# Kernel optimization log

Measured on AMD Instinct MI355X. Metric: run time of the kernel, lower is better.

The kernel has to match this reference:

```python
import jax, jax.numpy as jnp
import numpy as np

EPS = 0.1        # entropic regularization (self.eps)
THRESH = 0.1     # convergence threshold on sum|u - u1| (self.thresh)
MAX_ITER = 100   # self.max_iter
K = 8            # num_neighbors in get_mask_matrix


def setup_inputs() -> dict:
    key = jax.random.key(0)
    k1, k2, k3 = jax.random.split(key, 3)
    B, N, M = 8, 3000, 3000
    mu = jax.random.uniform(k1, (B, N), dtype=jnp.float32)
    mu = mu / mu.sum(-1, keepdims=True)
    nu = jax.random.uniform(k2, (B, M), dtype=jnp.float32)
    nu = nu / nu.sum(-1, keepdims=True)
    C = jax.random.uniform(k3, (B, N, M), dtype=jnp.float32)
    return {"mu": mu, "nu": nu, "C": C}


def _knn_mask(C, k=K):
    # get_mask_matrix: k smallest per row (dim=1) + k largest per column (dim=0)
    B, N, M = C.shape
    _, ir = jax.lax.top_k(-C, k)                       # [B,N,k] smallest along cols
    row_mask = jnp.zeros(C.shape, C.dtype).at[
        jnp.arange(B)[:, None, None], jnp.arange(N)[None, :, None], ir].set(1.0)
    _, ic = jax.lax.top_k(jnp.swapaxes(C, -1, -2), k)  # [B,M,k] largest along rows
    col_mask = jnp.zeros(C.shape, C.dtype).at[
        jnp.arange(B)[:, None, None], ic, jnp.arange(M)[None, :, None]].set(1.0)
    return ((row_mask + col_mask) > 0).astype(C.dtype)


def _sinkhorn(mu, nu, C, A):
    # log-domain Sinkhorn of get_dist, vectorized over batch with per-sample early stop
    B = mu.shape[0]
    log_mu = jnp.log(mu + 1e-8)
    log_nu = jnp.log(nu + 1e-8)

    def exp_M(u, v):
        return A * jnp.exp((-C + u[:, :, None] + v[:, None, :]) / EPS)

    def step(carry, _):
        u, v, done = carry
        u_new = EPS * (log_mu - jnp.log(1e-8 + exp_M(u, v).sum(-1))) + u
        v_new = EPS * (log_nu - jnp.log(1e-8 + exp_M(u_new, v).sum(-2))) + v
        err = jnp.abs(u_new - u).sum(-1)               # [B]
        u_out = jnp.where(done[:, None], u, u_new)
        v_out = jnp.where(done[:, None], v, v_new)
        done = done | (err < THRESH)
        return (u_out, v_out, done), None

    init = (jnp.zeros_like(mu), jnp.zeros_like(nu), jnp.zeros((B,), dtype=bool))
    (u, v, _), _ = jax.lax.scan(step, init, None, length=MAX_ITER)
    pi = exp_M(u, v)
    return jnp.sum(pi * C, axis=(-2, -1))              # [B]


def reference(mu, nu, C):
    # get_cost_matrix: row-wise L2 normalization (F.normalize p=2 dim=1)
    Cn = C / jnp.maximum(jnp.linalg.norm(C, axis=-1, keepdims=True), 1e-12)
    A = _knn_mask(Cn)
    Cm = A * Cn                                        # C = A.to_dense() * C
    cost = _sinkhorn(mu, nu, Cm, A)
    return cost.mean()                                 # gwd / batch
```

## Files before the change

kernel.cpp:

```cpp
#include <hip/hip_runtime.h>
#include <cfloat>

typedef unsigned long long ull;

constexpr int NB = 8, NN = 3000, NM = 3000, KK = 8;
constexpr int CAP = 48;
constexpr float SCALE   = 14.426950408889634f;
constexpr float UNSCALE = 0.06931471805599453f;
constexpr float THRESH  = 0.1f;
constexpr unsigned DUMMY_PAT = 0x7f7f7f7fu;
constexpr int RCH = 8;

constexpr int BPB  = 8;
constexpr int NBLK = NB * BPB;
constexpr int TPB  = 512;
constexpr int RPB  = NN / BPB;

#if __has_builtin(__builtin_amdgcn_exp2f)
#define FEXP2(x) __builtin_amdgcn_exp2f(x)
#else
#define FEXP2(x) exp2f(x)
#endif
#if __has_builtin(__builtin_amdgcn_logf)
#define FLOG2(x) __builtin_amdgcn_logf(x)
#else
#define FLOG2(x) __log2f(x)
#endif

__device__ __forceinline__ ull aload64(const ull* p) {
  return __hip_atomic_load(p, __ATOMIC_RELAXED, __HIP_MEMORY_SCOPE_AGENT);
}
__device__ __forceinline__ void astore64(ull* p, ull x) {
  __hip_atomic_store(p, x, __ATOMIC_RELAXED, __HIP_MEMORY_SCOPE_AGENT);
}

__device__ __forceinline__ void pull_tagged(const ull* __restrict__ src, int tag,
                                            float* __restrict__ dst, int lane) {
  const int nfull = RPB - 5 * 64;
  unsigned pend = (lane < nfull) ? 0x3Fu : 0x1Fu;
  {
    ull x0 = aload64(&src[lane]);
    ull x1 = aload64(&src[lane + 64]);
    ull x2 = aload64(&src[lane + 128]);
    ull x3 = aload64(&src[lane + 192]);
    ull x4 = aload64(&src[lane + 256]);
    ull x5 = (lane < nfull) ? aload64(&src[lane + 320]) : 0;
    if ((int)(x0 >> 32) == tag) { dst[lane]       = __uint_as_float((unsigned)x0); pend &= ~1u;  }
    if ((int)(x1 >> 32) == tag) { dst[lane + 64]  = __uint_as_float((unsigned)x1); pend &= ~2u;  }
    if ((int)(x2 >> 32) == tag) { dst[lane + 128] = __uint_as_float((unsigned)x2); pend &= ~4u;  }
    if ((int)(x3 >> 32) == tag) { dst[lane + 192] = __uint_as_float((unsigned)x3); pend &= ~8u;  }
    if ((int)(x4 >> 32) == tag) { dst[lane + 256] = __uint_as_float((unsigned)x4); pend &= ~16u; }
    if ((lane < nfull) && (int)(x5 >> 32) == tag) { dst[lane + 320] = __uint_as_float((unsigned)x5); pend &= ~32u; }
  }
  while (pend) {
    __builtin_amdgcn_s_sleep(1);
#pragma unroll
    for (int j = 0; j < 6; ++j) {
      if (!((pend >> j) & 1u)) continue;
      ull x = aload64(&src[lane + 64 * j]);
      if ((int)(x >> 32) == tag) {
        dst[lane + 64 * j] = __uint_as_float((unsigned)x);
        pend &= ~(1u << j);
      }
    }
  }
}

__global__ __launch_bounds__(256) void k_rowprep(const float* __restrict__ C,
                                                 float* __restrict__ invnorms,
                                                 int* __restrict__ rowsel) {
  const int bn = blockIdx.x * 8 + (threadIdx.x >> 5);
  const int l  = threadIdx.x & 31;
  const float4* row4 = reinterpret_cast<const float4*>(C + (size_t)bn * NM);

  float tv[8]; int ti[8];
#pragma unroll
  for (int q = 0; q < 8; ++q) { tv[q] = FLT_MAX; ti[q] = 0x7fffffff; }
  float sq = 0.f;
  for (int c = 0; c < 24; ++c) {
    int i = l + 32 * c;
    if (i < NM / 4) {
      float4 f = row4[i];
      sq += f.x * f.x + f.y * f.y + f.z * f.z + f.w * f.w;
      float e[4] = { f.x, f.y, f.z, f.w };
#pragma unroll
      for (int j = 0; j < 4; ++j) {
        float v = e[j];
        if (v < tv[7]) {
          int idx = 4 * i + j;
          int pos = 8;
#pragma unroll
          for (int q = 7; q >= 0; --q) if (v < tv[q]) pos = q;
#pragma unroll
          for (int q = 7; q >= 1; --q) if (q > pos) { tv[q] = tv[q-1]; ti[q] = ti[q-1]; }
#pragma unroll
          for (int q = 0; q < 8; ++q) if (q == pos) { tv[q] = v; ti[q] = idx; }
        }
      }
    }
  }
#pragma unroll
  for (int o = 16; o; o >>= 1) sq += __shfl_down(sq, o, 32);

#pragma unroll
  for (int msk = 1; msk <= 16; msk <<= 1) {
    float pv[8]; int pi[8];
#pragma unroll
    for (int q = 0; q < 8; ++q) { pv[q] = __shfl_xor(tv[q], msk); pi[q] = __shfl_xor(ti[q], msk); }
    float mv[8]; int mi[8];
#pragma unroll
    for (int q = 0; q < 8; ++q) {
      float av = tv[q], bv = pv[7 - q];
      int   ai = ti[q], bi = pi[7 - q];
      bool ta = (av < bv) || (av == bv && ai < bi);
      mv[q] = ta ? av : bv; mi[q] = ta ? ai : bi;
    }
    auto ce = [&](int i, int j) {
      bool sw = (mv[i] > mv[j]) || (mv[i] == mv[j] && mi[i] > mi[j]);
      float fv = sw ? mv[j] : mv[i], gv = sw ? mv[i] : mv[j];
      int   fi = sw ? mi[j] : mi[i], gi = sw ? mi[i] : mi[j];
      mv[i] = fv; mv[j] = gv; mi[i] = fi; mi[j] = gi;
    };
    ce(0,4); ce(1,5); ce(2,6); ce(3,7);
    ce(0,2); ce(1,3); ce(4,6); ce(5,7);
    ce(0,1); ce(2,3); ce(4,5); ce(6,7);
#pragma unroll
    for (int q = 0; q < 8; ++q) { tv[q] = mv[q]; ti[q] = mi[q]; }
  }

  if (l == 0) {
#pragma unroll
    for (int q = 0; q < 8; ++q) rowsel[(size_t)bn * KK + q] = ti[q];
    float nm = sqrtf(sq);
    invnorms[bn] = 1.0f / fmaxf(nm, 1e-12f);
  }
}

__global__ __launch_bounds__(256) void k_coltop1(const float* __restrict__ C,
                                                 const float* __restrict__ invnorms,
                                                 int2* __restrict__ partial) {
  const int b = blockIdx.z, rc = blockIdx.y, cg = blockIdx.x;
  const int tid = threadIdx.x;
  const int w = tid >> 6, l = tid & 63;
  const int g4 = cg * 64 + l;
  __shared__ float sv[4][256][8];
  __shared__ int   si[4][256][8];

  float tv[4][8]; int ti[4][8];
#pragma unroll
  for (int j = 0; j < 4; ++j)
#pragma unroll
    for (int q = 0; q < 8; ++q) { tv[j][q] = -FLT_MAX; ti[j][q] = 0x7fffffff; }

  if (g4 < NM / 4) {
    const int base_r = rc * 375;
    const int r0 = base_r + w * 94;
    const int r1 = min(base_r + 375, r0 + 94);
    const float4* base = reinterpret_cast<const float4*>(
        C + (size_t)b * NN * NM) + g4;
    const float* ivn = invnorms + (size_t)b * NN;
    for (int n = r0; n < r1; ++n) {
      float4 f = base[(size_t)n * (NM / 4)];
      float iv = ivn[n];
      float e[4] = { f.x * iv, f.y * iv, f.z * iv, f.w * iv };
#pragma unroll
      for (int j = 0; j < 4; ++j) {
        float v = e[j];
        if (v > tv[j][7]) {
          int pos = 8;
#pragma unroll
          for (int q = 7; q >= 0; --q) if (v > tv[j][q]) pos = q;
#pragma unroll
          for (int q = 7; q >= 1; --q) if (q > pos) { tv[j][q] = tv[j][q-1]; ti[j][q] = ti[j][q-1]; }
#pragma unroll
          for (int q = 0; q < 8; ++q) if (q == pos) { tv[j][q] = v; ti[j][q] = n; }
        }
      }
    }
  }
#pragma unroll
  for (int j = 0; j < 4; ++j)
#pragma unroll
    for (int q = 0; q < 8; ++q) { sv[w][l * 4 + j][q] = tv[j][q]; si[w][l * 4 + j][q] = ti[j][q]; }
  __syncthreads();

  int m = cg * 256 + tid;
  if (m < NM) {
    int2* dst = partial + (((size_t)b * RCH + rc) * NM + m) * 8;
    unsigned used = 0;
    for (int p = 0; p < KK; ++p) {
      float bv = -FLT_MAX; int bi = 0x7fffffff; int bq = 0;
      for (int c = 0; c < 4; ++c)
        for (int q = 0; q < 8; ++q) {
          int bit = c * 8 + q;
          if ((used >> bit) & 1u) continue;
          float v = sv[c][tid][q];
          int   n = si[c][tid][q];
          if (v > bv || (v == bv && n < bi)) { bv = v; bi = n; bq = bit; }
        }
      used |= 1u << bq;
      dst[p] = make_int2(bi, __float_as_int(bv));
    }
  }
}

__global__ __launch_bounds__(256) void k_coltop2(const int2* __restrict__ partial,
                                                 int* __restrict__ colsel) {
  int t = blockIdx.x * 256 + threadIdx.x;
  if (t >= NB * NM) return;
  int b = t / NM, m = t % NM;
  int2 cand[RCH * 8];
  for (int rc = 0; rc < RCH; ++rc) {
    const int2* src = partial + (((size_t)b * RCH + rc) * NM + m) * 8;
    for (int q = 0; q < 8; ++q) cand[rc * 8 + q] = src[q];
  }
  ull used = 0;
  for (int p = 0; p < KK; ++p) {
    float bv = -FLT_MAX; int bi = 0x7fffffff; int bq = 0;
    for (int k = 0; k < RCH * 8; ++k) {
      if ((used >> k) & 1ull) continue;
      float v = __int_as_float(cand[k].y);
      int   n = cand[k].x;
      if (v > bv || (v == bv && n < bi)) { bv = v; bi = n; bq = k; }
    }
    used |= 1ull << bq;
    colsel[(size_t)t * KK + p] = bi;
  }
}

__global__ __launch_bounds__(256) void k_fill(const float* __restrict__ C,
    const float* __restrict__ invnorms, const int* __restrict__ rowsel,
    const int* __restrict__ colsel, int* r_cnt, int* c_cnt,
    int2* __restrict__ r_pk, int2* __restrict__ c_pk) {
  int t = blockIdx.x * 256 + threadIdx.x;
  if (t >= NB * NN * KK) return;
  int k = t % KK; int bn = t / KK;
  int b = bn / NN; int n = bn % NN;
  {
    int m = rowsel[t];
    float v2 = C[((size_t)b * NN + n) * NM + m] * invnorms[bn] * SCALE;
    r_pk[(size_t)bn * CAP + k] = make_int2(m, __float_as_int(v2));
  }
  {
    int m2 = n;
    int n2 = colsel[t];
    float v2 = C[((size_t)b * NN + n2) * NM + m2] * invnorms[(size_t)b * NN + n2] * SCALE;
    c_pk[(size_t)bn * CAP + k] = make_int2(n2, __float_as_int(v2));
  }
  int m = n;
  {
    int n3 = colsel[t];
    const int* rs = rowsel + ((size_t)b * NN + n3) * KK;
    bool dup = false;
#pragma unroll
    for (int q = 0; q < KK; ++q) dup |= (rs[q] == m);
    if (!dup) {
      int slot = 8 + atomicAdd(&r_cnt[(size_t)b * NN + n3], 1);
      if (slot < CAP) {
        float v2 = C[((size_t)b * NN + n3) * NM + m] * invnorms[(size_t)b * NN + n3] * SCALE;
        r_pk[((size_t)b * NN + n3) * CAP + slot] = make_int2(m, __float_as_int(v2));
      }
    }
  }
  {
    int n2 = m;
    int mm = rowsel[t];
    const int* cs = colsel + ((size_t)b * NM + mm) * KK;
    bool dup = false;
#pragma unroll
    for (int q = 0; q < KK; ++q) dup |= (cs[q] == n2);
    if (!dup) {
      int slot = 8 + atomicAdd(&c_cnt[(size_t)b * NM + mm], 1);
      if (slot < CAP) {
        float v2 = C[((size_t)b * NN + n2) * NM + mm] * invnorms[(size_t)b * NN + n2] * SCALE;
        c_pk[((size_t)b * NM + mm) * CAP + slot] = make_int2(n2, __float_as_int(v2));
      }
    }
  }
}

__global__ __launch_bounds__(TPB, 1) void k_sink_coop(
    const float* __restrict__ mu, const float* __restrict__ nu,
    const int2* __restrict__ r_pk, const int2* __restrict__ c_pk,
    ull* __restrict__ Upub, ull* __restrict__ Vpub,
    ull* errW, float* __restrict__ costpart) {
  const int blk = blockIdx.x;
  const int b = blk % NB, slice = blk / NB;
  const int tid = threadIdx.x;
  const int w = tid >> 6, lane = tid & 63;
  const int r = slice * RPB + tid;
  const bool has_r = (tid < RPB);

  float rval[CAP], cval[CAP];
  unsigned ridx[CAP / 2], cidx[CAP / 2];
  float u = 0.f, vv = 0.f, lmu = 0.f, lnu = 0.f;
  if (has_r) {
    const int2* rp = r_pk + ((size_t)b * NN + r) * CAP;
    const int2* cp = c_pk + ((size_t)b * NM + r) * CAP;
#pragma unroll
    for (int i = 0; i < CAP; i += 2) {
      int2 e0 = rp[i], e1 = rp[i + 1];
      rval[i] = __int_as_float(e0.y); rval[i + 1] = __int_as_float(e1.y);
      unsigned i0 = min((unsigned)e0.x & 0xFFFFu, (unsigned)(NN - 1));
      unsigned i1 = min((unsigned)e1.x & 0xFFFFu, (unsigned)(NN - 1));
      ridx[i / 2] = i0 | (i1 << 16);
      int2 f0 = cp[i], f1 = cp[i + 1];
      cval[i] = __int_as_float(f0.y); cval[i + 1] = __int_as_float(f1.y);
      unsigned j0 = min((unsigned)f0.x & 0xFFFFu, (unsigned)(NN - 1));
      unsigned j1 = min((unsigned)f1.x & 0xFFFFu, (unsigned)(NN - 1));
      cidx[i / 2] = j0 | (j1 << 16);
    }
    lmu = FLOG2(mu[(size_t)b * NN + r] + 1e-8f);
    lnu = FLOG2(nu[(size_t)b * NM + r] + 1e-8f);
  }

  __shared__ float XL[NN];
  __shared__ float sred[TPB / 64];
  __shared__ float errl[BPB];
  int itf = 0;
  bool done = false;

  for (int it = 0; it < 100; ++it) {
    if (it == 0) {
      for (int i = tid; i < NN; i += TPB) XL[i] = 0.f;
    } else {
      if (has_r) XL[r] = vv;
      if (w != slice) {
        const ull* src = Vpub + (size_t)((it - 1) & 1) * (NB * NN)
                       + (size_t)b * NN + (size_t)w * RPB;
        pull_tagged(src, it, XL + w * RPB, lane);
      }
    }
    __syncthreads();

    float errp = 0.f;
    if (has_r) {
      float s = 0.f;
#pragma unroll
      for (int i = 0; i < CAP; ++i) {
        int ix = (ridx[i >> 1] >> ((i & 1) * 16)) & 0xFFFF;
        s += FEXP2(u + XL[ix] - rval[i]);
      }
      float un = lmu - FLOG2(1e-8f + s) + u;
      errp = fabsf(un - u);
      u = un;
      astore64(&Upub[(size_t)(it & 1) * (NB * NN) + (size_t)b * NN + r],
               ((ull)(unsigned)(it + 1) << 32) | __float_as_uint(u));
    }
#pragma unroll
    for (int o = 32; o; o >>= 1) errp += __shfl_down(errp, o);
    if (lane == 0) sred[w] = errp;
    __syncthreads();
    if (tid == 0) {
      float e = sred[0] + sred[1] + sred[2] + sred[3]
              + sred[4] + sred[5] + sred[6] + sred[7];
      astore64(&errW[(size_t)((it & 1) * NB + b) * BPB * 16 + slice * 16],
               ((ull)(unsigned)(it + 1) << 32) | __float_as_uint(e));
      errl[slice] = e;
    }

    if (has_r) XL[r] = u;
    if (w != slice) {
      const ull* src = Upub + (size_t)(it & 1) * (NB * NN)
                     + (size_t)b * NN + (size_t)w * RPB;
      pull_tagged(src, it + 1, XL + w * RPB, lane);
      if (lane == 0) {
        const ull* ep = errW + (size_t)((it & 1) * NB + b) * BPB * 16 + w * 16;
        ull x = aload64(ep);
        while ((int)(x >> 32) != it + 1) { __builtin_amdgcn_s_sleep(1); x = aload64(ep); }
        errl[w] = __uint_as_float((unsigned)x);
      }
    }
    __syncthreads();

    float errtot = errl[0] + errl[1] + errl[2] + errl[3]
                 + errl[4] + errl[5] + errl[6] + errl[7];
    done = (errtot * UNSCALE < THRESH);
    if (has_r) {
      float s = 0.f;
#pragma unroll
      for (int i = 0; i < CAP; ++i) {
        int ix = (cidx[i >> 1] >> ((i & 1) * 16)) & 0xFFFF;
        s += FEXP2(vv + XL[ix] - cval[i]);
      }
      vv = lnu - FLOG2(1e-8f + s) + vv;
      astore64(&Vpub[(size_t)(it & 1) * (NB * NN) + (size_t)b * NN + r],
               ((ull)(unsigned)(it + 1) << 32) | __float_as_uint(vv));
    }
    __syncthreads();
    itf = it;
    if (done) break;
  }

  if (has_r) XL[r] = vv;
  if (w != slice) {
    const ull* src = Vpub + (size_t)(itf & 1) * (NB * NN)
                   + (size_t)b * NN + (size_t)w * RPB;
    pull_tagged(src, itf + 1, XL + w * RPB, lane);
  }
  __syncthreads();
  float cs = 0.f;
  if (has_r) {
#pragma unroll
    for (int i = 0; i < CAP; ++i) {
      int ix = (ridx[i >> 1] >> ((i & 1) * 16)) & 0xFFFF;
      float val = rval[i];
      cs += FEXP2(u + XL[ix] - val) * val;
    }
  }
#pragma unroll
  for (int o = 32; o; o >>= 1) cs += __shfl_down(cs, o);
  if (lane == 0) sred[w] = cs;
  __syncthreads();
  if (tid == 0)
    costpart[b * BPB + slice] = sred[0] + sred[1] + sred[2] + sred[3]
                              + sred[4] + sred[5] + sred[6] + sred[7];
}

__global__ void k_final2(const float* __restrict__ costpart, float* __restrict__ out) {
  if (threadIdx.x == 0 && blockIdx.x == 0) {
    float tot = 0.f;
    for (int b = 0; b < NB; ++b) {
      float cb = 0.f;
      for (int s = 0; s < BPB; ++s) cb += costpart[b * BPB + s];
      tot += cb * UNSCALE;
    }
    out[0] = tot * (1.0f / NB);
  }
}

extern "C" void kernel_launch(void* const* d_in, const int* in_sizes, int n_in,
                              void* d_out, int out_size, void* d_ws, size_t ws_size,
                              hipStream_t stream) {
  const float* mu = (const float*)d_in[0];
  const float* nu = (const float*)d_in[1];
  const float* C  = (const float*)d_in[2];
  float* out = (float*)d_out;

  char* ws = (char*)d_ws;
  size_t off = 0;
  auto alloc = [&](size_t bytes) {
    void* p = ws + off;
    off += (bytes + 255) & ~(size_t)255;
    return p;
  };
  float* invnorms = (float*)alloc(sizeof(float) * NB * NN);
  int*   rowsel   = (int*)  alloc(sizeof(int)   * NB * NN * KK);
  int*   colsel   = (int*)  alloc(sizeof(int)   * NB * NM * KK);
  int2*  partial  = (int2*) alloc(sizeof(int2)  * NB * RCH * NM * 8);
  int2*  r_pk     = (int2*) alloc(sizeof(int2)  * NB * NN * CAP);
  int2*  c_pk     = (int2*) alloc(sizeof(int2)  * NB * NM * CAP);
  ull*   Upub     = (ull*)  alloc(sizeof(ull)   * 2 * NB * NN);
  ull*   Vpub     = (ull*)  alloc(sizeof(ull)   * 2 * NB * NM);
  ull*   errW     = (ull*)  alloc(sizeof(ull)   * 2 * NB * BPB * 16);
  int*   r_cnt    = (int*)  alloc(sizeof(int)   * NB * NN);
  int*   c_cnt    = (int*)  alloc(sizeof(int)   * NB * NM);
  float* costpart = (float*)alloc(sizeof(float) * NB * BPB);
  (void)ws_size; (void)in_sizes; (void)n_in; (void)out_size;

  hipMemsetD32Async((hipDeviceptr_t)r_pk, (int)DUMMY_PAT,
                    (size_t)2 * NB * NN * CAP * 2, stream);
  size_t span = (size_t)((char*)costpart - (char*)Upub)
              + ((sizeof(float) * NB * BPB + 255) & ~(size_t)255);
  hipMemsetAsync(Upub, 0, span, stream);

  hipLaunchKernelGGL(k_rowprep, dim3(NB * NN / 8), dim3(256), 0, stream,
                     C, invnorms, rowsel);
  hipLaunchKernelGGL(k_coltop1, dim3(12, RCH, NB), dim3(256), 0, stream,
                     C, invnorms, partial);
  hipLaunchKernelGGL(k_coltop2, dim3((NB * NM + 255) / 256), dim3(256), 0, stream,
                     partial, colsel);
  int nthreads = NB * NN * KK;
  hipLaunchKernelGGL(k_fill, dim3((nthreads + 255) / 256), dim3(256), 0, stream,
                     C, invnorms, rowsel, colsel, r_cnt, c_cnt, r_pk, c_pk);

  void* args[] = { (void*)&mu, (void*)&nu, (void*)&r_pk, (void*)&c_pk,
                   (void*)&Upub, (void*)&Vpub, (void*)&errW, (void*)&costpart };
  hipLaunchCooperativeKernel((const void*)k_sink_coop, dim3(NBLK), dim3(TPB),
                             args, 0, stream);

  hipLaunchKernelGGL(k_final2, dim3(1), dim3(64), 0, stream, costpart, out);
}
```

Baseline: 951.1 us.

## Pack top-k values with indices and drop shared-memory merge in column selection

```diff
diff --git a/kernel.cpp b/kernel.cpp
--- a/kernel.cpp
+++ b/kernel.cpp
@@ -9,7 +9,7 @@
 constexpr float UNSCALE = 0.06931471805599453f;
 constexpr float THRESH  = 0.1f;
 constexpr unsigned DUMMY_PAT = 0x7f7f7f7fu;
-constexpr int RCH = 8;
+constexpr int NCH = 32;
 
 constexpr int BPB  = 8;
 constexpr int NBLK = NB * BPB;
@@ -68,7 +68,7 @@
 
 __global__ __launch_bounds__(256) void k_rowprep(const float* __restrict__ C,
                                                  float* __restrict__ invnorms,
-                                                 int* __restrict__ rowsel) {
+                                                 int2* __restrict__ rowsel) {
   const int bn = blockIdx.x * 8 + (threadIdx.x >> 5);
   const int l  = threadIdx.x & 31;
   const float4* row4 = reinterpret_cast<const float4*>(C + (size_t)bn * NM);
@@ -130,7 +130,8 @@
 
   if (l == 0) {
 #pragma unroll
-    for (int q = 0; q < 8; ++q) rowsel[(size_t)bn * KK + q] = ti[q];
+    for (int q = 0; q < 8; ++q)
+      rowsel[(size_t)bn * KK + q] = make_int2(ti[q], __float_as_int(tv[q]));
     float nm = sqrtf(sq);
     invnorms[bn] = 1.0f / fmaxf(nm, 1e-12f);
   }
@@ -138,19 +139,18 @@
 
 __global__ __launch_bounds__(256) void k_coltop1(const float* __restrict__ C,
                                                  const float* __restrict__ invnorms,
-                                                 int2* __restrict__ partial) {
+                                                 ull* __restrict__ partial) {
   const int b = blockIdx.z, rc = blockIdx.y, cg = blockIdx.x;
   const int tid = threadIdx.x;
   const int w = tid >> 6, l = tid & 63;
   const int g4 = cg * 64 + l;
-  __shared__ float sv[4][256][8];
-  __shared__ int   si[4][256][8];
-
-  float tv[4][8]; int ti[4][8];
+  const int chunk = rc * 4 + w;
+
+  ull tv[4][8];
 #pragma unroll
   for (int j = 0; j < 4; ++j)
 #pragma unroll
-    for (int q = 0; q < 8; ++q) { tv[j][q] = -FLT_MAX; ti[j][q] = 0x7fffffff; }
+    for (int q = 0; q < 8; ++q) tv[j][q] = 0;
 
   if (g4 < NM / 4) {
     const int base_r = rc * 375;
@@ -163,117 +163,104 @@
       float4 f = base[(size_t)n * (NM / 4)];
       float iv = ivn[n];
       float e[4] = { f.x * iv, f.y * iv, f.z * iv, f.w * iv };
+      ull lo = (ull)(unsigned)~n;
 #pragma unroll
       for (int j = 0; j < 4; ++j) {
-        float v = e[j];
-        if (v > tv[j][7]) {
+        ull key = ((ull)__float_as_uint(e[j]) << 32) | lo;
+        if (key > tv[j][7]) {
           int pos = 8;
 #pragma unroll
-          for (int q = 7; q >= 0; --q) if (v > tv[j][q]) pos = q;
-#pragma unroll
-          for (int q = 7; q >= 1; --q) if (q > pos) { tv[j][q] = tv[j][q-1]; ti[j][q] = ti[j][q-1]; }
-#pragma unroll
-          for (int q = 0; q < 8; ++q) if (q == pos) { tv[j][q] = v; ti[j][q] = n; }
+          for (int q = 7; q >= 0; --q) if (key > tv[j][q]) pos = q;
+#pragma unroll
+          for (int q = 7; q >= 1; --q) if (q > pos) tv[j][q] = tv[j][q-1];
+#pragma unroll
+          for (int q = 0; q < 8; ++q) if (q == pos) tv[j][q] = key;
         }
       }
     }
-  }
-#pragma unroll
-  for (int j = 0; j < 4; ++j)
-#pragma unroll
-    for (int q = 0; q < 8; ++q) { sv[w][l * 4 + j][q] = tv[j][q]; si[w][l * 4 + j][q] = ti[j][q]; }
-  __syncthreads();
-
-  int m = cg * 256 + tid;
-  if (m < NM) {
-    int2* dst = partial + (((size_t)b * RCH + rc) * NM + m) * 8;
-    unsigned used = 0;
-    for (int p = 0; p < KK; ++p) {
-      float bv = -FLT_MAX; int bi = 0x7fffffff; int bq = 0;
-      for (int c = 0; c < 4; ++c)
-        for (int q = 0; q < 8; ++q) {
-          int bit = c * 8 + q;
-          if ((used >> bit) & 1u) continue;
-          float v = sv[c][tid][q];
-          int   n = si[c][tid][q];
-          if (v > bv || (v == bv && n < bi)) { bv = v; bi = n; bq = bit; }
-        }
-      used |= 1u << bq;
-      dst[p] = make_int2(bi, __float_as_int(bv));
-    }
-  }
-}
-
-__global__ __launch_bounds__(256) void k_coltop2(const int2* __restrict__ partial,
-                                                 int* __restrict__ colsel) {
+    ull* dst = partial + (((size_t)b * NCH + chunk) * NM + (size_t)4 * g4) * 8;
+#pragma unroll
+    for (int j = 0; j < 4; ++j)
+#pragma unroll
+      for (int q = 0; q < 8; ++q) dst[j * 8 + q] = tv[j][q];
+  }
+}
+
+__global__ __launch_bounds__(256) void k_coltop2(const ull* __restrict__ partial,
+                                                 int2* __restrict__ colsel) {
   int t = blockIdx.x * 256 + threadIdx.x;
   if (t >= NB * NM) return;
   int b = t / NM, m = t % NM;
-  int2 cand[RCH * 8];
-  for (int rc = 0; rc < RCH; ++rc) {
-    const int2* src = partial + (((size_t)b * RCH + rc) * NM + m) * 8;
-    for (int q = 0; q < 8; ++q) cand[rc * 8 + q] = src[q];
-  }
-  ull used = 0;
-  for (int p = 0; p < KK; ++p) {
-    float bv = -FLT_MAX; int bi = 0x7fffffff; int bq = 0;
-    for (int k = 0; k < RCH * 8; ++k) {
-      if ((used >> k) & 1ull) continue;
-      float v = __int_as_float(cand[k].y);
-      int   n = cand[k].x;
-      if (v > bv || (v == bv && n < bi)) { bv = v; bi = n; bq = k; }
-    }
-    used |= 1ull << bq;
-    colsel[(size_t)t * KK + p] = bi;
-  }
-}
-
-__global__ __launch_bounds__(256) void k_fill(const float* __restrict__ C,
-    const float* __restrict__ invnorms, const int* __restrict__ rowsel,
-    const int* __restrict__ colsel, int* r_cnt, int* c_cnt,
-    int2* __restrict__ r_pk, int2* __restrict__ c_pk) {
+  ull top[8];
+#pragma unroll
+  for (int q = 0; q < 8; ++q) top[q] = 0;
+  for (int c = 0; c < NCH; ++c) {
+    const ull* src = partial + (((size_t)b * NCH + c) * NM + m) * 8;
+    ull buf[8];
+#pragma unroll
+    for (int q = 0; q < 8; ++q) buf[q] = src[q];
+    for (int q = 0; q < 8; ++q) {
+      ull key = buf[q];
+      if (key <= top[7]) break;
+      int pos = 8;
+#pragma unroll
+      for (int z = 7; z >= 0; --z) if (key > top[z]) pos = z;
+#pragma unroll
+      for (int z = 7; z >= 1; --z) if (z > pos) top[z] = top[z-1];
+#pragma unroll
+      for (int z = 0; z < 8; ++z) if (z == pos) top[z] = key;
+    }
+  }
+#pragma unroll
+  for (int q = 0; q < 8; ++q)
+    colsel[(size_t)t * KK + q] =
+        make_int2((int)~(unsigned)top[q], (int)(top[q] >> 32));
+}
+
+__global__ __launch_bounds__(256) void k_fill(const float* __restrict__ invnorms,
+    const int2* __restrict__ rowsel, const int2* __restrict__ colsel,
+    int* r_cnt, int* c_cnt, int2* __restrict__ r_pk, int2* __restrict__ c_pk) {
   int t = blockIdx.x * 256 + threadIdx.x;
   if (t >= NB * NN * KK) return;
   int k = t % KK; int bn = t / KK;
   int b = bn / NN; int n = bn % NN;
+  float inv_bn = invnorms[bn];
+  int2 rs = rowsel[t];
+  int2 cs = colsel[t];
   {
-    int m = rowsel[t];
-    float v2 = C[((size_t)b * NN + n) * NM + m] * invnorms[bn] * SCALE;
-    r_pk[(size_t)bn * CAP + k] = make_int2(m, __float_as_int(v2));
+    float v2 = __int_as_float(rs.y) * inv_bn * SCALE;
+    r_pk[(size_t)bn * CAP + k] = make_int2(rs.x, __float_as_int(v2));
   }
   {
-    int m2 = n;
-    int n2 = colsel[t];
-    float v2 = C[((size_t)b * NN + n2) * NM + m2] * invnorms[(size_t)b * NN + n2] * SCALE;
-    c_pk[(size_t)bn * CAP + k] = make_int2(n2, __float_as_int(v2));
+    float v2 = __int_as_float(cs.y) * SCALE;
+    c_pk[(size_t)bn * CAP + k] = make_int2(cs.x, __float_as_int(v2));
   }
   int m = n;
   {
-    int n3 = colsel[t];
-    const int* rs = rowsel + ((size_t)b * NN + n3) * KK;
+    int n3 = cs.x;
+    const int2* rl = rowsel + ((size_t)b * NN + n3) * KK;
     bool dup = false;
 #pragma unroll
-    for (int q = 0; q < KK; ++q) dup |= (rs[q] == m);
+    for (int q = 0; q < KK; ++q) dup |= (rl[q].x == m);
     if (!dup) {
       int slot = 8 + atomicAdd(&r_cnt[(size_t)b * NN + n3], 1);
       if (slot < CAP) {
-        float v2 = C[((size_t)b * NN + n3) * NM + m] * invnorms[(size_t)b * NN + n3] * SCALE;
+        float v2 = __int_as_float(cs.y) * SCALE;
         r_pk[((size_t)b * NN + n3) * CAP + slot] = make_int2(m, __float_as_int(v2));
       }
     }
   }
   {
-    int n2 = m;
-    int mm = rowsel[t];
-    const int* cs = colsel + ((size_t)b * NM + mm) * KK;
+    int mm = rs.x;
+    const int2* cl = colsel + ((size_t)b * NM + mm) * KK;
     bool dup = false;
 #pragma unroll
-    for (int q = 0; q < KK; ++q) dup |= (cs[q] == n2);
+    for (int q = 0; q < KK; ++q) dup |= (cl[q].x == n);
     if (!dup) {
       int slot = 8 + atomicAdd(&c_cnt[(size_t)b * NM + mm], 1);
       if (slot < CAP) {
-        float v2 = C[((size_t)b * NN + n2) * NM + mm] * invnorms[(size_t)b * NN + n2] * SCALE;
-        c_pk[((size_t)b * NM + mm) * CAP + slot] = make_int2(n2, __float_as_int(v2));
+        float v2 = __int_as_float(rs.y) * inv_bn * SCALE;
+        c_pk[((size_t)b * NM + mm) * CAP + slot] = make_int2(n, __float_as_int(v2));
       }
     }
   }
@@ -445,9 +432,9 @@
     return p;
   };
   float* invnorms = (float*)alloc(sizeof(float) * NB * NN);
-  int*   rowsel   = (int*)  alloc(sizeof(int)   * NB * NN * KK);
-  int*   colsel   = (int*)  alloc(sizeof(int)   * NB * NM * KK);
-  int2*  partial  = (int2*) alloc(sizeof(int2)  * NB * RCH * NM * 8);
+  int2*  rowsel   = (int2*) alloc(sizeof(int2)  * NB * NN * KK);
+  int2*  colsel   = (int2*) alloc(sizeof(int2)  * NB * NM * KK);
+  ull*   partial  = (ull*)  alloc(sizeof(ull)   * NB * NCH * NM * 8);
   int2*  r_pk     = (int2*) alloc(sizeof(int2)  * NB * NN * CAP);
   int2*  c_pk     = (int2*) alloc(sizeof(int2)  * NB * NM * CAP);
   ull*   Upub     = (ull*)  alloc(sizeof(ull)   * 2 * NB * NN);
@@ -466,13 +453,13 @@
 
   hipLaunchKernelGGL(k_rowprep, dim3(NB * NN / 8), dim3(256), 0, stream,
                      C, invnorms, rowsel);
-  hipLaunchKernelGGL(k_coltop1, dim3(12, RCH, NB), dim3(256), 0, stream,
+  hipLaunchKernelGGL(k_coltop1, dim3(12, NCH / 4, NB), dim3(256), 0, stream,
                      C, invnorms, partial);
   hipLaunchKernelGGL(k_coltop2, dim3((NB * NM + 255) / 256), dim3(256), 0, stream,
                      partial, colsel);
   int nthreads = NB * NN * KK;
   hipLaunchKernelGGL(k_fill, dim3((nthreads + 255) / 256), dim3(256), 0, stream,
-                     C, invnorms, rowsel, colsel, r_cnt, c_cnt, r_pk, c_pk);
+                     invnorms, rowsel, colsel, r_cnt, c_cnt, r_pk, c_pk);
 
   void* args[] = { (void*)&mu, (void*)&nu, (void*)&r_pk, (void*)&c_pk,
                    (void*)&Upub, (void*)&Vpub, (void*)&errW, (void*)&costpart };
```

After: 831.9 us. -12.5%, faster.
